# Kernel tuning notes

Measured on AMD Instinct MI355X. Metric: run time of the kernel, lower is better.

Reference implementation:

```python
import jax, jax.numpy as jnp
import numpy as np

N_NODES = 8192
EMBED = 64
HID = [256, 256, 128]
ACTION = 8192


def setup_inputs() -> dict:
    key = jax.random.key(0)
    ks = jax.random.split(key, 16)
    state = jax.random.uniform(ks[0], (N_NODES, N_NODES), dtype=jnp.float32)
    start = 100  # python int node index
    def u(k, shape, fan_out):
        s = 1.0 / np.sqrt(fan_out)
        return jax.random.uniform(k, shape, minval=-s, maxval=s, dtype=jnp.float32)
    def xav(k, shape):
        s = np.sqrt(6.0 / (shape[0] + shape[1]))
        return jax.random.uniform(k, shape, minval=-s, maxval=s, dtype=jnp.float32)
    in_size = N_NODES + EMBED
    return {
        "state": state,
        "start": start,
        "gc1_w": u(ks[1], (1, HID[0]), HID[0]),
        "gc1_b": u(ks[2], (HID[0],), HID[0]),
        "gc2_w": u(ks[3], (HID[0], EMBED), EMBED),
        "gc2_b": u(ks[4], (EMBED,), EMBED),
        "fc1_w": xav(ks[5], (HID[0], in_size)),
        "fc1_b": jnp.zeros((HID[0],), jnp.float32),
        "fc2_w": xav(ks[6], (HID[1], HID[0])),
        "fc2_b": jnp.zeros((HID[1],), jnp.float32),
        "fc3_w": xav(ks[7], (HID[2], HID[1])),
        "fc3_b": jnp.zeros((HID[2],), jnp.float32),
        "fc4_w": xav(ks[8], (ACTION, HID[2])),
        "fc4_b": jnp.zeros((ACTION,), jnp.float32),
    }


def reference(state, start, gc1_w, gc1_b, gc2_w, gc2_b,
              fc1_w, fc1_b, fc2_w, fc2_b, fc3_w, fc3_b, fc4_w, fc4_b):
    n = state.shape[0]
    # node features = diagonal of state, shape [N, 1]
    x = jnp.diagonal(state)[:, None]
    # adjacency: state with zeroed diagonal, detached (no grad to state via adj)
    idx = jnp.arange(n)
    adj = jax.lax.stop_gradient(state.at[idx, idx].set(0.0))
    # GCN layer 1: spmm(adj, x @ W) + b, relu  (dropout inactive: eval mode)
    h = jax.nn.relu(adj @ (x @ gc1_w) + gc1_b)          # [N, 256]
    # GCN layer 2
    h = jax.nn.relu(adj @ (h @ gc2_w) + gc2_b)          # [N, 64]
    h = jax.nn.log_softmax(h, axis=1)
    start_embedding = h[start]                           # [64]
    start_features = state[start, :]                     # [N]
    e = jnp.concatenate([start_features, start_embedding], axis=-1)  # [N+64]
    y = jax.nn.relu(e @ fc1_w.T + fc1_b)
    y = jax.nn.relu(y @ fc2_w.T + fc2_b)
    y = jax.nn.relu(y @ fc3_w.T + fc3_b)
    end_q = jax.nn.relu(y @ fc4_w.T + fc4_b)             # [action_size]
    return end_q
```

## Files before the change

### kernel.cpp

```cpp
#include <hip/hip_runtime.h>

#define NODES 8192
#define H1 256
#define EMB 64
#define IN_SIZE (NODES + EMB)
#define HID3 128

#define X_OFF    0
#define M_OFF    (X_OFF + NODES)
#define PART_OFF (M_OFF + NODES*EMB)
#define LS_OFF   (PART_OFF + 256*EMB)
#define Y1_OFF   (LS_OFF + EMB)
#define Y3_OFF   (Y1_OFF + H1)

__device__ __forceinline__ float waveReduceSum(float v) {
    #pragma unroll
    for (int off = 32; off > 0; off >>= 1) v += __shfl_down(v, off, 64);
    return v;
}

__global__ __launch_bounds__(256) void k_diag(const float* __restrict__ state,
                                              float* __restrict__ x) {
    int i = blockIdx.x * 256 + threadIdx.x;
    x[i] = state[(size_t)i * NODES + i];
}

__global__ __launch_bounds__(256) void k_row(const float* __restrict__ state,
                                             const float* __restrict__ x,
                                             const float* __restrict__ w1,
                                             const float* __restrict__ b1,
                                             const float* __restrict__ w2,
                                             float* __restrict__ M) {
    __shared__ float red[4];
    __shared__ float s_bcast;
    __shared__ float h1[H1];
    __shared__ float mp[4][EMB];

    const int i = blockIdx.x;
    const int tid = threadIdx.x;
    const float4* row4 = (const float4*)(state + (size_t)i * NODES);
    const float4* x4   = (const float4*)x;

    float acc = 0.f;
    #pragma unroll
    for (int it = 0; it < NODES / 4 / 256; ++it) {
        int j = tid + it * 256;
        float4 r = row4[j];
        float4 xv = x4[j];
        acc += r.x * xv.x + r.y * xv.y + r.z * xv.z + r.w * xv.w;
    }
    acc = waveReduceSum(acc);
    if ((tid & 63) == 0) red[tid >> 6] = acc;
    __syncthreads();
    if (tid == 0) {
        float s = red[0] + red[1] + red[2] + red[3];
        float xi = x[i];
        s_bcast = s - xi * xi;
    }
    __syncthreads();
    const float s = s_bcast;

    h1[tid] = fmaxf(s * w1[tid] + b1[tid], 0.f);
    __syncthreads();

    const int k = tid & 63, g = tid >> 6;
    float m = 0.f;
    #pragma unroll
    for (int jj = 0; jj < 64; ++jj) {
        int j = g * 64 + jj;
        m += h1[j] * w2[j * EMB + k];
    }
    mp[g][k] = m;
    __syncthreads();
    if (tid < EMB)
        M[(size_t)i * EMB + tid] = mp[0][tid] + mp[1][tid] + mp[2][tid] + mp[3][tid];
}

__global__ __launch_bounds__(256) void k_colpart(const float* __restrict__ state,
                                                 const int* __restrict__ pstart,
                                                 const float* __restrict__ M,
                                                 float* __restrict__ part) {
    __shared__ float mp[4][EMB];
    const int start = *pstart;
    const int b = blockIdx.x;
    const int t = threadIdx.x;
    const int k = t & 63, g = t >> 6;
    const float* srow = state + (size_t)start * NODES;
    float acc = 0.f;
    #pragma unroll
    for (int r = 0; r < 8; ++r) {
        int i = b * 32 + g + r * 4;
        float coef = (i == start) ? 0.f : srow[i];
        acc += coef * M[(size_t)i * EMB + k];
    }
    mp[g][k] = acc;
    __syncthreads();
    if (t < EMB) part[b * EMB + t] = mp[0][t] + mp[1][t] + mp[2][t] + mp[3][t];
}

__global__ __launch_bounds__(256) void k_softmax(const float* __restrict__ part,
                                                 const float* __restrict__ b2,
                                                 float* __restrict__ ls) {
    __shared__ float mp[4][EMB];
    const int t = threadIdx.x;
    const int k = t & 63, g = t >> 6;
    float acc = 0.f;
    #pragma unroll
    for (int c = 0; c < 64; ++c) acc += part[(g * 64 + c) * EMB + k];
    mp[g][k] = acc;
    __syncthreads();
    if (t < 64) {
        float v = mp[0][k] + mp[1][k] + mp[2][k] + mp[3][k];
        v = fmaxf(v + b2[k], 0.f);
        float mx = v;
        #pragma unroll
        for (int off = 32; off; off >>= 1) mx = fmaxf(mx, __shfl_xor(mx, off, 64));
        float e = expf(v - mx);
        float se = e;
        #pragma unroll
        for (int off = 32; off; off >>= 1) se += __shfl_xor(se, off, 64);
        ls[k] = (v - mx) - logf(se);
    }
}

__global__ __launch_bounds__(256) void k_fc1(const float* __restrict__ state,
                                             const int* __restrict__ pstart,
                                             const float* __restrict__ ls,
                                             const float* __restrict__ w,
                                             const float* __restrict__ b,
                                             float* __restrict__ y1) {
    __shared__ float red[4];
    const int o = blockIdx.x;
    const int t = threadIdx.x;
    const int start = *pstart;
    const float4* e4 = (const float4*)(state + (size_t)start * NODES);
    const float4* w4 = (const float4*)(w + (size_t)o * IN_SIZE);
    float acc = 0.f;
    #pragma unroll
    for (int it = 0; it < 8; ++it) {
        int j = t + it * 256;
        float4 a = e4[j], ww = w4[j];
        acc += a.x * ww.x + a.y * ww.y + a.z * ww.z + a.w * ww.w;
    }
    if (t < 64) acc += ls[t] * w[(size_t)o * IN_SIZE + NODES + t];
    acc = waveReduceSum(acc);
    if ((t & 63) == 0) red[t >> 6] = acc;
    __syncthreads();
    if (t == 0) y1[o] = fmaxf(red[0] + red[1] + red[2] + red[3] + b[o], 0.f);
}

__global__ __launch_bounds__(256) void k_fc23(const float* __restrict__ y1,
                                              const float* __restrict__ w2_,
                                              const float* __restrict__ b2_,
                                              const float* __restrict__ w3_,
                                              const float* __restrict__ b3_,
                                              float* __restrict__ y3) {
    __shared__ float ly[H1];
    __shared__ float ly2[H1];
    const int t = threadIdx.x;
    ly[t] = y1[t];
    __syncthreads();
    const float4* w4 = (const float4*)(w2_ + (size_t)t * H1);
    float acc = 0.f;
    #pragma unroll
    for (int j = 0; j < 64; ++j) {
        float4 ww = w4[j];
        acc += ww.x * ly[j*4] + ww.y * ly[j*4+1] + ww.z * ly[j*4+2] + ww.w * ly[j*4+3];
    }
    ly2[t] = fmaxf(acc + b2_[t], 0.f);
    __syncthreads();
    if (t < HID3) {
        const float4* w43 = (const float4*)(w3_ + (size_t)t * H1);
        float a3 = 0.f;
        #pragma unroll
        for (int j = 0; j < 64; ++j) {
            float4 ww = w43[j];
            a3 += ww.x * ly2[j*4] + ww.y * ly2[j*4+1] + ww.z * ly2[j*4+2] + ww.w * ly2[j*4+3];
        }
        y3[t] = fmaxf(a3 + b3_[t], 0.f);
    }
}

__global__ __launch_bounds__(256) void k_fc4(const float* __restrict__ y3,
                                             const float* __restrict__ w,
                                             const float* __restrict__ b,
                                             float* __restrict__ out) {
    __shared__ float ly[HID3];
    const int t = threadIdx.x;
    if (t < HID3) ly[t] = y3[t];
    __syncthreads();
    const int wave = t >> 6, lane = t & 63;
    const int o = blockIdx.x * 4 + wave;
    const float* wr = w + (size_t)o * HID3;
    float acc = wr[lane] * ly[lane] + wr[64 + lane] * ly[64 + lane];
    acc = waveReduceSum(acc);
    if (lane == 0) out[o] = fmaxf(acc + b[o], 0.f);
}

extern "C" void kernel_launch(void* const* d_in, const int* in_sizes, int n_in,
                              void* d_out, int out_size, void* d_ws, size_t ws_size,
                              hipStream_t stream) {
    const float* state = (const float*)d_in[0];
    const int*   pstart= (const int*)  d_in[1];
    const float* gc1_w = (const float*)d_in[2];
    const float* gc1_b = (const float*)d_in[3];
    const float* gc2_w = (const float*)d_in[4];
    const float* gc2_b = (const float*)d_in[5];
    const float* fc1_w = (const float*)d_in[6];
    const float* fc1_b = (const float*)d_in[7];
    const float* fc2_w = (const float*)d_in[8];
    const float* fc2_b = (const float*)d_in[9];
    const float* fc3_w = (const float*)d_in[10];
    const float* fc3_b = (const float*)d_in[11];
    const float* fc4_w = (const float*)d_in[12];
    const float* fc4_b = (const float*)d_in[13];
    float* ws = (float*)d_ws;
    float* x    = ws + X_OFF;
    float* M    = ws + M_OFF;
    float* part = ws + PART_OFF;
    float* ls   = ws + LS_OFF;
    float* y1   = ws + Y1_OFF;
    float* y3   = ws + Y3_OFF;
    float* out  = (float*)d_out;

    k_diag   <<<NODES / 256, 256, 0, stream>>>(state, x);
    k_row    <<<NODES,       256, 0, stream>>>(state, x, gc1_w, gc1_b, gc2_w, M);
    k_colpart<<<256,         256, 0, stream>>>(state, pstart, M, part);
    k_softmax<<<1,           256, 0, stream>>>(part, gc2_b, ls);
    k_fc1    <<<H1,          256, 0, stream>>>(state, pstart, ls, fc1_w, fc1_b, y1);
    k_fc23   <<<1,           256, 0, stream>>>(y1, fc2_w, fc2_b, fc3_w, fc3_b, y3);
    k_fc4    <<<8192 / 4,    256, 0, stream>>>(y3, fc4_w, fc4_b, out);
}
```

Before: 422.1 us.

## Defer gc2 projection until after node aggregation to drop per-row matvec

```diff
diff --git a/kernel.cpp b/kernel.cpp
--- a/kernel.cpp
+++ b/kernel.cpp
@@ -5,11 +5,12 @@
 #define EMB 64
 #define IN_SIZE (NODES + EMB)
 #define HID3 128
+#define NPART 256
 
 #define X_OFF    0
-#define M_OFF    (X_OFF + NODES)
-#define PART_OFF (M_OFF + NODES*EMB)
-#define LS_OFF   (PART_OFF + 256*EMB)
+#define S_OFF    (X_OFF + NODES)
+#define PART_OFF (S_OFF + NODES)
+#define LS_OFF   (PART_OFF + NPART*H1)
 #define Y1_OFF   (LS_OFF + EMB)
 #define Y3_OFF   (Y1_OFF + H1)
 
@@ -27,15 +28,8 @@
 
 __global__ __launch_bounds__(256) void k_row(const float* __restrict__ state,
                                              const float* __restrict__ x,
-                                             const float* __restrict__ w1,
-                                             const float* __restrict__ b1,
-                                             const float* __restrict__ w2,
-                                             float* __restrict__ M) {
+                                             float* __restrict__ s) {
     __shared__ float red[4];
-    __shared__ float s_bcast;
-    __shared__ float h1[H1];
-    __shared__ float mp[4][EMB];
-
     const int i = blockIdx.x;
     const int tid = threadIdx.x;
     const float4* row4 = (const float4*)(state + (size_t)i * NODES);
@@ -53,73 +47,59 @@
     if ((tid & 63) == 0) red[tid >> 6] = acc;
     __syncthreads();
     if (tid == 0) {
-        float s = red[0] + red[1] + red[2] + red[3];
         float xi = x[i];
-        s_bcast = s - xi * xi;
-    }
-    __syncthreads();
-    const float s = s_bcast;
-
-    h1[tid] = fmaxf(s * w1[tid] + b1[tid], 0.f);
-    __syncthreads();
-
-    const int k = tid & 63, g = tid >> 6;
-    float m = 0.f;
-    #pragma unroll
-    for (int jj = 0; jj < 64; ++jj) {
-        int j = g * 64 + jj;
-        m += h1[j] * w2[j * EMB + k];
-    }
-    mp[g][k] = m;
-    __syncthreads();
-    if (tid < EMB)
-        M[(size_t)i * EMB + tid] = mp[0][tid] + mp[1][tid] + mp[2][tid] + mp[3][tid];
-}
-
-__global__ __launch_bounds__(256) void k_colpart(const float* __restrict__ state,
-                                                 const int* __restrict__ pstart,
-                                                 const float* __restrict__ M,
-                                                 float* __restrict__ part) {
-    __shared__ float mp[4][EMB];
+        s[i] = red[0] + red[1] + red[2] + red[3] - xi * xi;
+    }
+}
+
+__global__ __launch_bounds__(256) void k_tpart(const float* __restrict__ s,
+                                               const float* __restrict__ state,
+                                               const int* __restrict__ pstart,
+                                               const float* __restrict__ w1,
+                                               const float* __restrict__ b1,
+                                               float* __restrict__ part) {
+    __shared__ float ls_s[32], ls_a[32];
+    const int b = blockIdx.x, t = threadIdx.x;
     const int start = *pstart;
-    const int b = blockIdx.x;
-    const int t = threadIdx.x;
-    const int k = t & 63, g = t >> 6;
-    const float* srow = state + (size_t)start * NODES;
-    float acc = 0.f;
-    #pragma unroll
-    for (int r = 0; r < 8; ++r) {
-        int i = b * 32 + g + r * 4;
-        float coef = (i == start) ? 0.f : srow[i];
-        acc += coef * M[(size_t)i * EMB + k];
-    }
-    mp[g][k] = acc;
-    __syncthreads();
-    if (t < EMB) part[b * EMB + t] = mp[0][t] + mp[1][t] + mp[2][t] + mp[3][t];
-}
-
-__global__ __launch_bounds__(256) void k_softmax(const float* __restrict__ part,
-                                                 const float* __restrict__ b2,
-                                                 float* __restrict__ ls) {
-    __shared__ float mp[4][EMB];
-    const int t = threadIdx.x;
-    const int k = t & 63, g = t >> 6;
-    float acc = 0.f;
-    #pragma unroll
-    for (int c = 0; c < 64; ++c) acc += part[(g * 64 + c) * EMB + k];
-    mp[g][k] = acc;
-    __syncthreads();
-    if (t < 64) {
-        float v = mp[0][k] + mp[1][k] + mp[2][k] + mp[3][k];
-        v = fmaxf(v + b2[k], 0.f);
-        float mx = v;
+    if (t < 32) {
+        int i = b * 32 + t;
+        ls_s[t] = s[i];
+        float a = state[(size_t)start * NODES + i];
+        ls_a[t] = (i == start) ? 0.f : a;
+    }
+    __syncthreads();
+    const float w = w1[t], bb = b1[t];
+    float acc = 0.f;
+    #pragma unroll
+    for (int q = 0; q < 32; ++q)
+        acc += ls_a[q] * fmaxf(ls_s[q] * w + bb, 0.f);
+    part[b * H1 + t] = acc;
+}
+
+__global__ __launch_bounds__(256) void k_sm(const float* __restrict__ part,
+                                            const float* __restrict__ w2,
+                                            const float* __restrict__ b2,
+                                            float* __restrict__ ls) {
+    __shared__ float ts[H1];
+    const int t = threadIdx.x;
+    float acc = 0.f;
+    #pragma unroll 8
+    for (int b = 0; b < NPART; ++b) acc += part[b * H1 + t];
+    ts[t] = acc;
+    __syncthreads();
+    if (t < EMB) {
+        float u = 0.f;
+        #pragma unroll 8
+        for (int j = 0; j < H1; ++j) u += ts[j] * w2[j * EMB + t];
+        u = fmaxf(u + b2[t], 0.f);
+        float mx = u;
         #pragma unroll
         for (int off = 32; off; off >>= 1) mx = fmaxf(mx, __shfl_xor(mx, off, 64));
-        float e = expf(v - mx);
+        float e = expf(u - mx);
         float se = e;
         #pragma unroll
         for (int off = 32; off; off >>= 1) se += __shfl_xor(se, off, 64);
-        ls[k] = (v - mx) - logf(se);
+        ls[t] = (u - mx) - logf(se);
     }
 }
 
@@ -216,18 +196,18 @@
     const float* fc4_b = (const float*)d_in[13];
     float* ws = (float*)d_ws;
     float* x    = ws + X_OFF;
-    float* M    = ws + M_OFF;
+    float* s    = ws + S_OFF;
     float* part = ws + PART_OFF;
     float* ls   = ws + LS_OFF;
     float* y1   = ws + Y1_OFF;
     float* y3   = ws + Y3_OFF;
     float* out  = (float*)d_out;
 
-    k_diag   <<<NODES / 256, 256, 0, stream>>>(state, x);
-    k_row    <<<NODES,       256, 0, stream>>>(state, x, gc1_w, gc1_b, gc2_w, M);
-    k_colpart<<<256,         256, 0, stream>>>(state, pstart, M, part);
-    k_softmax<<<1,           256, 0, stream>>>(part, gc2_b, ls);
-    k_fc1    <<<H1,          256, 0, stream>>>(state, pstart, ls, fc1_w, fc1_b, y1);
-    k_fc23   <<<1,           256, 0, stream>>>(y1, fc2_w, fc2_b, fc3_w, fc3_b, y3);
-    k_fc4    <<<8192 / 4,    256, 0, stream>>>(y3, fc4_w, fc4_b, out);
-}
+    k_diag <<<NODES / 256, 256, 0, stream>>>(state, x);
+    k_row  <<<NODES,       256, 0, stream>>>(state, x, s);
+    k_tpart<<<NPART,       256, 0, stream>>>(s, state, pstart, gc1_w, gc1_b, part);
+    k_sm   <<<1,           256, 0, stream>>>(part, gc2_w, gc2_b, ls);
+    k_fc1  <<<H1,          256, 0, stream>>>(state, pstart, ls, fc1_w, fc1_b, y1);
+    k_fc23 <<<1,           256, 0, stream>>>(y1, fc2_w, fc2_b, fc3_w, fc3_b, y3);
+    k_fc4  <<<8192 / 4,    256, 0, stream>>>(y3, fc4_w, fc4_b, out);
+}
```

Measured after the change: 435.4 us, median of 2. 3.2% more time.
